# Performance work log

Hardware: AMD Instinct MI355X
Metric: run time of the kernel (lower is better)

## Reference

```python
import jax, jax.numpy as jnp
import numpy as np
from functools import partial

B, L = 8, 2500          # batch, note length
V = 50002               # vocab + 2
E = 100                 # embed_size
F = 50                  # num_filter_maps
K = 9                   # kernel_size (padding = 4)
Y = 8922                # number of ICD codes (Y4)


def setup_inputs() -> dict:
    key = jax.random.key(0)
    ks = jax.random.split(key, 12)
    x = jax.random.randint(ks[0], (B, L), 0, 50000, dtype=jnp.int64)
    target = jnp.zeros((B, Y), dtype=jnp.float32)
    embed_w = jax.random.normal(ks[1], (V, E), dtype=jnp.float32) * 0.1
    embed_w = embed_w.at[0].set(0.0)  # padding_idx=0
    conv_w = jax.random.normal(ks[2], (F, E, K), dtype=jnp.float32) * (1.0 / np.sqrt(E * K))
    conv_b = jnp.zeros((F,), dtype=jnp.float32)
    U4_w = jax.random.normal(ks[3], (Y, F), dtype=jnp.float32) * (1.0 / np.sqrt(F))
    gcn_w = jax.random.normal(ks[4], (F, F), dtype=jnp.float32) * (1.0 / np.sqrt(F))
    gcn_b = jax.random.uniform(ks[5], (F,), dtype=jnp.float32, minval=-1/np.sqrt(F), maxval=1/np.sqrt(F))
    # normalized co-occurrence adjacency (row-stochastic-ish, fixed buffer)
    adj = jax.random.uniform(ks[6], (Y, Y), dtype=jnp.float32)
    adj = adj / jnp.sum(adj, axis=1, keepdims=True)
    final4t_w = jax.random.normal(ks[7], (Y, F), dtype=jnp.float32) * (1.0 / np.sqrt(F))
    final4t_b = jnp.zeros((Y,), dtype=jnp.float32)
    final4_w = jax.random.normal(ks[8], (Y, 2 * F), dtype=jnp.float32) * (1.0 / np.sqrt(2 * F))
    final4_b = jnp.zeros((Y,), dtype=jnp.float32)
    return {
        "x": x, "target": target,
        "embed_w": embed_w, "conv_w": conv_w, "conv_b": conv_b,
        "U4_w": U4_w, "gcn_w": gcn_w, "gcn_b": gcn_b, "adj": adj,
        "final4t_w": final4t_w, "final4t_b": final4t_b,
        "final4_w": final4_w, "final4_b": final4_b,
    }


def reference(x, target, embed_w, conv_w, conv_b, U4_w, gcn_w, gcn_b, adj,
              final4t_w, final4t_b, final4_w, final4_b):
    # embedding (dropout is identity at inference)
    emb = embed_w[x]                              # [B, L, E]
    # conv1d over sequence: NCH layout, same padding
    h = jax.lax.conv_general_dilated(
        emb.transpose(0, 2, 1), conv_w,
        window_strides=(1,), padding=[(K // 2, K // 2)],
        dimension_numbers=("NCH", "OIH", "NCH"))
    hp = jnp.tanh(h.transpose(0, 2, 1) + conv_b)  # [B, L, F]
    # per-label attention over sequence
    scores = jnp.einsum("yf,blf->byl", U4_w, hp)  # [B, Y, L]
    alpha4 = jax.nn.softmax(scores, axis=-1)
    m4t = jnp.einsum("byl,blf->byf", alpha4, hp)  # [B, Y, F]
    # graph conv over label co-occurrence graph
    support = jnp.einsum("byf,fg->byg", m4t, gcn_w)
    out1 = jnp.einsum("yz,bzg->byg", adj, support) + gcn_b
    out1 = jax.nn.leaky_relu(out1, negative_slope=0.2)
    m4 = jnp.concatenate([m4t, out1], axis=2)     # [B, Y, 2F]
    # label-wise linear scoring
    y4t = jnp.einsum("byf,yf->by", m4t, final4t_w) + final4t_b
    y4 = jnp.einsum("byf,yf->by", m4, final4_w) + final4_b
    return y4t, y4
```

## Files before the change

### kernel.cpp

```cpp
#include <hip/hip_runtime.h>

typedef unsigned short u16;
typedef short bf16x8 __attribute__((ext_vector_type(8)));
typedef float f32x4  __attribute__((ext_vector_type(4)));
typedef u16   u16x8  __attribute__((ext_vector_type(8)));

#define MFMA_BF16(a, b, c) __builtin_amdgcn_mfma_f32_16x16x32_bf16((a), (b), (c), 0, 0, 0)

#define B_  8
#define L_  2500
#define LP  2528
#define E_  100
#define F_  50
#define Y_  8922
#define YP  8960
#define KT_ 280
#define NT_ 416
#define KP_ 3
#define AMAX_ (Y_ * Y_ - 1)

__device__ __forceinline__ u16 f2bf(float f) {
    unsigned int x = __float_as_uint(f);
    unsigned int r = x + 0x7fffu + ((x >> 16) & 1u);
    return (u16)(r >> 16);
}

__device__ __forceinline__ void glds16(const void* g, const void* l) {
    __builtin_amdgcn_global_load_lds(
        (const __attribute__((address_space(1))) unsigned int*)(unsigned long long)g,
        (__attribute__((address_space(3))) unsigned int*)(unsigned int)(unsigned long long)l,
        16, 0, 0);
}
__device__ __forceinline__ void glds4(const void* g, const void* l) {
    __builtin_amdgcn_global_load_lds(
        (const __attribute__((address_space(1))) unsigned int*)(unsigned long long)g,
        (__attribute__((address_space(3))) unsigned int*)(unsigned int)(unsigned long long)l,
        4, 0, 0);
}

__global__ __launch_bounds__(256) void k0_prep(
    const int* __restrict__ x, const float* __restrict__ conv_w,
    int* __restrict__ flag, float* __restrict__ wT)
{
    const int k = blockIdx.x;
    const int tid = threadIdx.x;
    if (k == 0 && tid == 0) {
        int nz = 0;
        #pragma unroll
        for (int i = 0; i < 32; i++) nz |= x[2 * i + 1];
        *flag = (nz == 0) ? 1 : 0;
    }
    for (int j = tid; j < 5000; j += 256)
        wT[k * 5000 + j] = conv_w[j * 9 + k];
}

__global__ __launch_bounds__(256) void k1_conv(
    const int* __restrict__ x, const int* __restrict__ flag,
    const float* __restrict__ embed_w, const float* __restrict__ wT,
    const float* __restrict__ conv_b,
    u16* __restrict__ hp, u16* __restrict__ hpT)
{
    __shared__ float sEmb[72 * 108];
    __shared__ int   sId[72];
    const int tid = threadIdx.x;
    const int b  = blockIdx.y;
    const int l0 = blockIdx.x * 64;
    const int is64 = *flag;

    if (tid < 72) {
        int l = l0 - 4 + tid;
        int id = -1;
        if (l >= 0 && l < L_) id = is64 ? x[(b * L_ + l) * 2] : x[b * L_ + l];
        sId[tid] = id;
    }
    __syncthreads();
    for (int i = tid; i < 72 * 25; i += 256) {
        int r = i / 25, e4 = i - r * 25;
        int id = sId[r];
        float4 v = make_float4(0.f, 0.f, 0.f, 0.f);
        if (id >= 0) v = *(const float4*)&embed_w[(size_t)id * 100 + e4 * 4];
        *(float4*)&sEmb[r * 108 + e4 * 4] = v;
    }
    __syncthreads();

    const int li = tid & 63;
    const int fg = __builtin_amdgcn_readfirstlane(tid >> 6);

    int fidx[13];
    #pragma unroll
    for (int i = 0; i < 13; i++) { int f = fg + 4 * i; fidx[i] = (f < F_) ? f : 49; }

    float acc[13];
    #pragma unroll
    for (int i = 0; i < 13; i++) { int f = fg + 4 * i; acc[i] = (f < F_) ? conv_b[f] : 0.f; }

    for (int k = 0; k < 9; k++) {
        const float* wk = wT + k * 5000;
        for (int e4 = 0; e4 < 25; e4++) {
            float4 h = *(const float4*)&sEmb[(li + k) * 108 + e4 * 4];
            #pragma unroll
            for (int i = 0; i < 13; i++) {
                float4 w = *(const float4*)&wk[fidx[i] * 100 + e4 * 4];
                acc[i] += h.x * w.x + h.y * w.y + h.z * w.z + h.w * w.w;
            }
        }
    }

    int l = l0 + li;
    if (l < LP) {
        bool valid = (l < L_);
        #pragma unroll
        for (int i = 0; i < 13; i++) {
            int f = fg + 4 * i;
            if (f < F_) {
                u16 hv = 0;
                if (valid) {
                    float e2 = __expf(2.f * acc[i]);
                    hv = f2bf((e2 - 1.f) / (e2 + 1.f));
                }
                hp [((size_t)b * LP + l) * 64 + f] = hv;
                hpT[((size_t)b * 64 + f) * LP + l] = hv;
            }
        }
        #pragma unroll
        for (int j = 0; j < 4; j++) {
            int f = 50 + fg + 4 * j;
            if (f < 64) {
                hp [((size_t)b * LP + l) * 64 + f] = 0;
                hpT[((size_t)b * 64 + f) * LP + l] = (f == 50 && valid) ? f2bf(1.f) : (u16)0;
            }
        }
    }
}

__global__ __launch_bounds__(256) void k2_attn(
    const float* __restrict__ U4_w,
    const u16* __restrict__ hp, const u16* __restrict__ hpT,
    float* __restrict__ m4t)
{
    __shared__ u16  sU4[128 * 72];
    __shared__ u16  sHp[32 * 72];
    __shared__ u16  sHt[64 * 40];
    __shared__ u16  sP [128 * 40];
    __shared__ float sDen[128];

    const int tid  = threadIdx.x;
    const int b    = blockIdx.y;
    const int y0   = blockIdx.x * 128;
    const int w    = tid >> 6;
    const int lane = tid & 63;
    const int l15  = lane & 15;
    const int quad = lane >> 4;

    for (int i = tid; i < 128 * 72; i += 256) {
        int r = i / 72, c = i - r * 72;
        float v = 0.f;
        int y = y0 + r;
        if (c < F_ && y < Y_) v = U4_w[y * F_ + c];
        sU4[i] = f2bf(v);
    }
    __syncthreads();

    bf16x8 fa[2][2];
    #pragma unroll
    for (int mi = 0; mi < 2; mi++)
        #pragma unroll
        for (int ks = 0; ks < 2; ks++)
            fa[mi][ks] = *(const bf16x8*)&sU4[(w * 32 + mi * 16 + l15) * 72 + ks * 32 + quad * 8];

    const f32x4 fz = {0.f, 0.f, 0.f, 0.f};
    f32x4 pacc[2][4];
    #pragma unroll
    for (int mi = 0; mi < 2; mi++)
        #pragma unroll
        for (int ni = 0; ni < 4; ni++) pacc[mi][ni] = fz;

    const int rr = tid >> 3, seg = tid & 7;
    const int fr = tid >> 2, s2 = tid & 3;
    u16x8 pv, pv2;
    {
        pv  = *(const u16x8*)&hp [((size_t)b * LP + rr) * 64 + seg * 8];
        pv2 = *(const u16x8*)&hpT[((size_t)b * 64 + fr) * LP + s2 * 8];
    }

    for (int lt = 0; lt < 79; lt++) {
        const int l0 = lt * 32;
        __syncthreads();
        *(u16x8*)&sHp[rr * 72 + seg * 8] = pv;
        *(u16x8*)&sHt[fr * 40 + s2 * 8] = pv2;
        if (lt + 1 < 79) {
            const int ln = l0 + 32;
            pv  = *(const u16x8*)&hp [((size_t)b * LP + ln + rr) * 64 + seg * 8];
            pv2 = *(const u16x8*)&hpT[((size_t)b * 64 + fr) * LP + ln + s2 * 8];
        }
        __syncthreads();

        f32x4 sacc[2][2];
        #pragma unroll
        for (int mi = 0; mi < 2; mi++)
            #pragma unroll
            for (int ni = 0; ni < 2; ni++) sacc[mi][ni] = fz;
        #pragma unroll
        for (int ks = 0; ks < 2; ks++) {
            #pragma unroll
            for (int ni = 0; ni < 2; ni++) {
                bf16x8 fb = *(const bf16x8*)&sHp[(ni * 16 + l15) * 72 + ks * 32 + quad * 8];
                #pragma unroll
                for (int mi = 0; mi < 2; mi++)
                    sacc[mi][ni] = MFMA_BF16(fa[mi][ks], fb, sacc[mi][ni]);
            }
        }
        #pragma unroll
        for (int mi = 0; mi < 2; mi++)
            #pragma unroll
            for (int ni = 0; ni < 2; ni++) {
                int lcol = ni * 16 + l15;
                bool lv = (l0 + lcol) < L_;
                #pragma unroll
                for (int r = 0; r < 4; r++) {
                    float p = lv ? __expf(sacc[mi][ni][r]) : 0.f;
                    sP[(w * 32 + mi * 16 + quad * 4 + r) * 40 + lcol] = f2bf(p);
                }
            }
        asm volatile("s_waitcnt lgkmcnt(0)" ::: "memory");
        __builtin_amdgcn_sched_barrier(0);

        bf16x8 fv[4];
        #pragma unroll
        for (int ni = 0; ni < 4; ni++)
            fv[ni] = *(const bf16x8*)&sHt[(ni * 16 + l15) * 40 + quad * 8];
        #pragma unroll
        for (int mi = 0; mi < 2; mi++) {
            bf16x8 fp_ = *(const bf16x8*)&sP[(w * 32 + mi * 16 + l15) * 40 + quad * 8];
            #pragma unroll
            for (int ni = 0; ni < 4; ni++)
                pacc[mi][ni] = MFMA_BF16(fp_, fv[ni], pacc[mi][ni]);
        }
    }

    if (l15 == 2) {
        #pragma unroll
        for (int mi = 0; mi < 2; mi++)
            #pragma unroll
            for (int r = 0; r < 4; r++)
                sDen[w * 32 + mi * 16 + quad * 4 + r] = pacc[mi][3][r];
    }
    __syncthreads();

    #pragma unroll
    for (int mi = 0; mi < 2; mi++)
        #pragma unroll
        for (int ni = 0; ni < 4; ni++) {
            int f = ni * 16 + l15;
            if (f < F_) {
                #pragma unroll
                for (int r = 0; r < 4; r++) {
                    int yl = w * 32 + mi * 16 + quad * 4 + r;
                    int y = y0 + yl;
                    if (y < Y_)
                        m4t[((size_t)b * Y_ + y) * F_ + f] = pacc[mi][ni][r] / sDen[yl];
                }
            }
        }
}

__global__ __launch_bounds__(256) void k3_support(
    const float* __restrict__ m4t, const float* __restrict__ gcn_w,
    const float* __restrict__ f4t_w, const float* __restrict__ f4t_b,
    u16* __restrict__ Bt, float* __restrict__ y4t_out)
{
    __shared__ float sW[50 * 52];
    const int tid = threadIdx.x;
    for (int i = tid; i < 50 * 52; i += 256) {
        int g = i / 52, f = i - g * 52;
        sW[i] = (f < F_) ? gcn_w[f * F_ + g] : 0.f;
    }
    __syncthreads();

    const int b = blockIdx.y;
    const int y = blockIdx.x * 256 + tid;
    if (y >= Y_) return;

    float2 m[25];
    const float* mrow = m4t + ((size_t)b * Y_ + y) * F_;
    #pragma unroll
    for (int i = 0; i < 25; i++) m[i] = *(const float2*)(mrow + 2 * i);

    const int kt = y >> 5, zo = y & 31;
    const int zhi = zo >> 3, zlo = zo & 7;
    u16* btile = Bt + (size_t)kt * (NT_ * 32);
    for (int g = 0; g < F_; g++) {
        float s = 0.f;
        const float* wr = sW + g * 52;
        #pragma unroll
        for (int i = 0; i < 25; i++) {
            float2 wv = *(const float2*)(wr + 2 * i);
            s += m[i].x * wv.x + m[i].y * wv.y;
        }
        int n = b * F_ + g;
        btile[n * 32 + ((zhi ^ ((n >> 1) & 3)) << 3) + zlo] = f2bf(s);
    }

    const float* tw = f4t_w + (size_t)y * F_;
    float acc = f4t_b[y];
    #pragma unroll
    for (int i = 0; i < 25; i++) {
        float2 wv = *(const float2*)(tw + 2 * i);
        acc += m[i].x * wv.x + m[i].y * wv.y;
    }
    y4t_out[(size_t)b * Y_ + y] = acc;
}

__global__ __launch_bounds__(512, 2) void k4_gemm(
    const float* __restrict__ adj, const u16* __restrict__ Bt,
    float* __restrict__ outp)
{
    __shared__ float sA[3][128 * 32];
    __shared__ u16   sB[2][NT_ * 32];

    const int tid  = threadIdx.x;
    const int bid  = blockIdx.x;
    const int kp   = bid % KP_;
    const int mIdx = bid / KP_;
    const int m0   = mIdx * 128;
    const int w    = tid >> 6;
    const int wq   = __builtin_amdgcn_readfirstlane(w);
    const int lane = tid & 63;
    const int l15  = lane & 15;
    const int quad = lane >> 4;
    const int wm   = w & 3;
    const int wn   = w >> 2;

    const int rA   = tid >> 5;
    const int colA = ((((tid & 31) >> 2) ^ (rA & 7)) << 2) | (tid & 3);
    const unsigned rbaseA = (unsigned)(m0 + rA) * (unsigned)Y_ + (unsigned)colA;

    const int r7    = l15 & 7;
    const int offA0 = (((2 * quad)     ^ r7) << 2);
    const int offA1 = (((2 * quad + 1) ^ r7) << 2);
    const int offB  = ((quad ^ ((l15 >> 1) & 3)) << 3);

    const f32x4 fz = {0.f, 0.f, 0.f, 0.f};
    f32x4 acc[2][13];
    #pragma unroll
    for (int mi = 0; mi < 2; mi++)
        #pragma unroll
        for (int ni = 0; ni < 13; ni++) acc[mi][ni] = fz;

    auto stageB = [&](int buf, int kt) {
        const char* bt = (const char*)Bt + (size_t)kt * (NT_ * 32 * 2);
        char* sb = (char*)sB[buf];
        #pragma unroll
        for (int j = 0; j < 3; j++)
            glds16(bt + j * 8192 + tid * 16, sb + j * 8192 + wq * 1024);
        glds4(bt + 24576 + tid * 4, sb + 24576 + wq * 256);
    };
    auto stageA = [&](int buf, int kt) {
        char* sa = (char*)sA[buf];
        const unsigned idx0 = rbaseA + (unsigned)kt * 32u;
        #pragma unroll
        for (int j = 0; j < 8; j++) {
            unsigned idx = idx0 + (unsigned)(j * 16 * Y_);
            idx = (idx > (unsigned)AMAX_) ? (unsigned)AMAX_ : idx;
            glds4(adj + idx, sa + j * 2048 + wq * 256);
        }
    };

    const int kt0   = (kp == 0) ? 0 : 1 + 93 * kp;
    const int niter = 93 + (kp == 0);
    const int ktmax = kt0 + niter - 1;
    stageB(0, kt0);
    stageA(0, kt0);
    stageA(1, kt0 + 1);

    int a0 = 0;
    for (int it = 0; it < niter; it++) {
        int ktb = kt0 + it + 1; if (ktb > ktmax) ktb = ktmax;
        int kta = kt0 + it + 2; if (kta > ktmax) kta = ktmax;
        stageB((it + 1) & 1, ktb);
        int a2 = a0 + 2; if (a2 >= 3) a2 -= 3;
        stageA(a2, kta);
        asm volatile("s_waitcnt vmcnt(20)" ::: "memory");
        __builtin_amdgcn_s_barrier();
        __builtin_amdgcn_sched_barrier(0);

        const float* sAc = sA[a0];
        const u16*   sBc = sB[it & 1];
        bf16x8 fa[2];
        #pragma unroll
        for (int mi = 0; mi < 2; mi++) {
            const int rb = (wm * 32 + mi * 16 + l15) * 32;
            f32x4 x0 = *(const f32x4*)&sAc[rb + offA0];
            f32x4 x1 = *(const f32x4*)&sAc[rb + offA1];
            bf16x8 v;
            v[0] = (short)f2bf(x0[0]); v[1] = (short)f2bf(x0[1]);
            v[2] = (short)f2bf(x0[2]); v[3] = (short)f2bf(x0[3]);
            v[4] = (short)f2bf(x1[0]); v[5] = (short)f2bf(x1[1]);
            v[6] = (short)f2bf(x1[2]); v[7] = (short)f2bf(x1[3]);
            fa[mi] = v;
        }
        #pragma unroll
        for (int ni = 0; ni < 13; ni++) {
            bf16x8 fb = *(const bf16x8*)&sBc[(wn * 208 + ni * 16 + l15) * 32 + offB];
            acc[0][ni] = MFMA_BF16(fa[0], fb, acc[0][ni]);
            acc[1][ni] = MFMA_BF16(fa[1], fb, acc[1][ni]);
        }

        __builtin_amdgcn_sched_barrier(0);
        asm volatile("s_waitcnt lgkmcnt(0)" ::: "memory");
        __builtin_amdgcn_s_barrier();
        __builtin_amdgcn_sched_barrier(0);
        a0++; if (a0 >= 3) a0 = 0;
    }
    asm volatile("s_waitcnt vmcnt(0)" ::: "memory");
    __builtin_amdgcn_sched_barrier(0);

    float* dst = outp + (size_t)kp * Y_ * 400;
    #pragma unroll
    for (int mi = 0; mi < 2; mi++)
        #pragma unroll
        for (int ni = 0; ni < 13; ni++) {
            int n = wn * 208 + ni * 16 + l15;
            if (n < 400) {
                #pragma unroll
                for (int r4 = 0; r4 < 4; r4++) {
                    int y = m0 + wm * 32 + mi * 16 + quad * 4 + r4;
                    if (y < Y_) dst[(size_t)y * 400 + n] = acc[mi][ni][r4];
                }
            }
        }
}

__global__ __launch_bounds__(256) void k5_final(
    const float* __restrict__ outp, const float* __restrict__ m4t,
    const float* __restrict__ gcn_b, const float* __restrict__ f4_w,
    const float* __restrict__ f4_b, float* __restrict__ y4_out)
{
    const int b = blockIdx.y;
    const int y = blockIdx.x * 256 + threadIdx.x;
    if (y >= Y_) return;

    const size_t PS = (size_t)Y_ * 400;
    const float* p0 = outp + (size_t)y * 400 + b * F_;
    const float* fw = f4_w + (size_t)y * 100;
    const float* mrow = m4t + ((size_t)b * Y_ + y) * F_;

    float acc = f4_b[y];
    #pragma unroll
    for (int i = 0; i < 25; i++) {
        float2 mv = *(const float2*)(mrow + 2 * i);
        float2 wv = *(const float2*)(fw + 2 * i);
        acc += mv.x * wv.x + mv.y * wv.y;
    }
    #pragma unroll
    for (int i = 0; i < 25; i++) {
        float sx = 0.f, sy = 0.f;
        #pragma unroll
        for (int kp = 0; kp < KP_; kp++) {
            float2 v = *(const float2*)(p0 + kp * PS + 2 * i);
            sx += v.x; sy += v.y;
        }
        float2 gb = *(const float2*)(gcn_b + 2 * i);
        sx += gb.x; sy += gb.y;
        sx = sx > 0.f ? sx : 0.2f * sx;
        sy = sy > 0.f ? sy : 0.2f * sy;
        float2 wv = *(const float2*)(fw + 50 + 2 * i);
        acc += sx * wv.x + sy * wv.y;
    }
    y4_out[(size_t)b * Y_ + y] = acc;
}

extern "C" void kernel_launch(void* const* d_in, const int* in_sizes, int n_in,
                              void* d_out, int out_size, void* d_ws, size_t ws_size,
                              hipStream_t stream) {
    const int*   x       = (const int*)d_in[0];
    const float* embed_w = (const float*)d_in[2];
    const float* conv_w  = (const float*)d_in[3];
    const float* conv_b  = (const float*)d_in[4];
    const float* U4_w    = (const float*)d_in[5];
    const float* gcn_w   = (const float*)d_in[6];
    const float* gcn_b   = (const float*)d_in[7];
    const float* adj     = (const float*)d_in[8];
    const float* f4t_w   = (const float*)d_in[9];
    const float* f4t_b   = (const float*)d_in[10];
    const float* f4_w    = (const float*)d_in[11];
    const float* f4_b    = (const float*)d_in[12];
    float* out = (float*)d_out;

    char* ws = (char*)d_ws;
    const size_t SZ_WT  = 180224;
    const size_t SZ_HP  = (size_t)B_ * LP * 64 * 2;
    const size_t SZ_BT  = (size_t)KT_ * NT_ * 32 * 2;
    const size_t SZ_M4T = (size_t)B_ * Y_ * F_ * 4;
    int*   flag = (int*)ws;
    float* wT   = (float*)(ws + 16);
    u16*   hp   = (u16*)(ws + 16 + SZ_WT);
    u16*   hpT  = (u16*)(ws + 16 + SZ_WT + SZ_HP);
    u16*   Bt   = (u16*)(ws + 16 + SZ_WT + 2 * SZ_HP);
    float* m4t  = (float*)(ws + 16 + SZ_WT + 2 * SZ_HP + SZ_BT);
    float* outp = (float*)(ws + 16 + SZ_WT + 2 * SZ_HP + SZ_BT + SZ_M4T);

    k0_prep<<<9, 256, 0, stream>>>(x, conv_w, flag, wT);
    k1_conv<<<dim3(40, 8), 256, 0, stream>>>(x, flag, embed_w, wT, conv_b, hp, hpT);
    hipMemsetAsync(Bt, 0, SZ_BT, stream);
    k2_attn<<<dim3(70, 8), 256, 0, stream>>>(U4_w, hp, hpT, m4t);
    k3_support<<<dim3(35, 8), 256, 0, stream>>>(m4t, gcn_w, f4t_w, f4t_b, Bt, out);
    k4_gemm<<<dim3(70 * KP_), 512, 0, stream>>>(adj, Bt, outp);
    k5_final<<<dim3(35, 8), 256, 0, stream>>>(outp, m4t, gcn_b, f4_w, f4_b,
                                              out + (size_t)B_ * Y_);
}
```

Before: 829.9 us.

## Double-buffer hp tiles in attention kernel and drop U4 shared staging

The attention kernel now double-buffers the hp and hpT tiles in shared memory, so each sequence tile needs one barrier instead of two. The U4 weight fragments are loaded straight from global memory into registers, which removes the 128x72 shared staging buffer and its barrier. s_setprio is raised around the MFMA sections. This cuts barrier stalls and LDS footprint, which may allow higher occupancy. The cost is uncoalesced per-lane scalar loads of U4 at kernel start and one extra tile of LDS.

```diff
diff --git a/kernel.cpp b/kernel.cpp
--- a/kernel.cpp
+++ b/kernel.cpp
@@ -138,9 +138,8 @@
     const u16* __restrict__ hp, const u16* __restrict__ hpT,
     float* __restrict__ m4t)
 {
-    __shared__ u16  sU4[128 * 72];
-    __shared__ u16  sHp[32 * 72];
-    __shared__ u16  sHt[64 * 40];
+    __shared__ u16  sHp[2][32 * 72];
+    __shared__ u16  sHt[2][64 * 40];
     __shared__ u16  sP [128 * 40];
     __shared__ float sDen[128];
 
@@ -152,21 +151,23 @@
     const int l15  = lane & 15;
     const int quad = lane >> 4;
 
-    for (int i = tid; i < 128 * 72; i += 256) {
-        int r = i / 72, c = i - r * 72;
-        float v = 0.f;
-        int y = y0 + r;
-        if (c < F_ && y < Y_) v = U4_w[y * F_ + c];
-        sU4[i] = f2bf(v);
-    }
-    __syncthreads();
-
     bf16x8 fa[2][2];
     #pragma unroll
-    for (int mi = 0; mi < 2; mi++)
-        #pragma unroll
-        for (int ks = 0; ks < 2; ks++)
-            fa[mi][ks] = *(const bf16x8*)&sU4[(w * 32 + mi * 16 + l15) * 72 + ks * 32 + quad * 8];
+    for (int mi = 0; mi < 2; mi++) {
+        int y = y0 + w * 32 + mi * 16 + l15;
+        #pragma unroll
+        for (int ks = 0; ks < 2; ks++) {
+            bf16x8 v;
+            #pragma unroll
+            for (int j = 0; j < 8; j++) {
+                int c = ks * 32 + quad * 8 + j;
+                float x = 0.f;
+                if (y < Y_ && c < F_) x = U4_w[(size_t)y * F_ + c];
+                v[j] = (short)f2bf(x);
+            }
+            fa[mi][ks] = v;
+        }
+    }
 
     const f32x4 fz = {0.f, 0.f, 0.f, 0.f};
     f32x4 pacc[2][4];
@@ -178,38 +179,48 @@
     const int rr = tid >> 3, seg = tid & 7;
     const int fr = tid >> 2, s2 = tid & 3;
     u16x8 pv, pv2;
+    pv  = *(const u16x8*)&hp [((size_t)b * LP + rr) * 64 + seg * 8];
+    pv2 = *(const u16x8*)&hpT[((size_t)b * 64 + fr) * LP + s2 * 8];
+    *(u16x8*)&sHp[0][rr * 72 + seg * 8] = pv;
+    *(u16x8*)&sHt[0][fr * 40 + s2 * 8] = pv2;
     {
-        pv  = *(const u16x8*)&hp [((size_t)b * LP + rr) * 64 + seg * 8];
-        pv2 = *(const u16x8*)&hpT[((size_t)b * 64 + fr) * LP + s2 * 8];
-    }
-
+        const int ln = 32;
+        pv  = *(const u16x8*)&hp [((size_t)b * LP + ln + rr) * 64 + seg * 8];
+        pv2 = *(const u16x8*)&hpT[((size_t)b * 64 + fr) * LP + ln + s2 * 8];
+    }
+
+    int cur = 0;
     for (int lt = 0; lt < 79; lt++) {
         const int l0 = lt * 32;
         __syncthreads();
-        *(u16x8*)&sHp[rr * 72 + seg * 8] = pv;
-        *(u16x8*)&sHt[fr * 40 + s2 * 8] = pv2;
-        if (lt + 1 < 79) {
-            const int ln = l0 + 32;
+
+        *(u16x8*)&sHp[cur ^ 1][rr * 72 + seg * 8] = pv;
+        *(u16x8*)&sHt[cur ^ 1][fr * 40 + s2 * 8] = pv2;
+        {
+            int lnext = lt + 2; if (lnext > 78) lnext = 78;
+            const int ln = lnext * 32;
             pv  = *(const u16x8*)&hp [((size_t)b * LP + ln + rr) * 64 + seg * 8];
             pv2 = *(const u16x8*)&hpT[((size_t)b * 64 + fr) * LP + ln + s2 * 8];
         }
-        __syncthreads();
 
         f32x4 sacc[2][2];
         #pragma unroll
         for (int mi = 0; mi < 2; mi++)
             #pragma unroll
             for (int ni = 0; ni < 2; ni++) sacc[mi][ni] = fz;
+        __builtin_amdgcn_s_setprio(1);
         #pragma unroll
         for (int ks = 0; ks < 2; ks++) {
             #pragma unroll
             for (int ni = 0; ni < 2; ni++) {
-                bf16x8 fb = *(const bf16x8*)&sHp[(ni * 16 + l15) * 72 + ks * 32 + quad * 8];
+                bf16x8 fb = *(const bf16x8*)&sHp[cur][(ni * 16 + l15) * 72 + ks * 32 + quad * 8];
                 #pragma unroll
                 for (int mi = 0; mi < 2; mi++)
                     sacc[mi][ni] = MFMA_BF16(fa[mi][ks], fb, sacc[mi][ni]);
             }
         }
+        __builtin_amdgcn_s_setprio(0);
+
         #pragma unroll
         for (int mi = 0; mi < 2; mi++)
             #pragma unroll
@@ -228,7 +239,8 @@
         bf16x8 fv[4];
         #pragma unroll
         for (int ni = 0; ni < 4; ni++)
-            fv[ni] = *(const bf16x8*)&sHt[(ni * 16 + l15) * 40 + quad * 8];
+            fv[ni] = *(const bf16x8*)&sHt[cur][(ni * 16 + l15) * 40 + quad * 8];
+        __builtin_amdgcn_s_setprio(1);
         #pragma unroll
         for (int mi = 0; mi < 2; mi++) {
             bf16x8 fp_ = *(const bf16x8*)&sP[(w * 32 + mi * 16 + l15) * 40 + quad * 8];
@@ -236,6 +248,8 @@
             for (int ni = 0; ni < 4; ni++)
                 pacc[mi][ni] = MFMA_BF16(fp_, fv[ni], pacc[mi][ni]);
         }
+        __builtin_amdgcn_s_setprio(0);
+        cur ^= 1;
     }
 
     if (l15 == 2) {
```

New measurement: 824.0 us. Within noise of the previous version (-0.7%).
